# Kernel optimization log

Measured on AMD Instinct MI355X. Metric: run time of the kernel, lower is better.

Reference implementation:

```python
import jax, jax.numpy as jnp
import numpy as np

B, T, D, H = 2, 2048, 2048, 16
HD = D // H  # head_dim = 128
ROPE_THETA = 10000.0


def _apply_rope_interleaved(x, cos, sin):
    # x: (B, T, H, HD); cos/sin: (1, T, 1, HD//2). rope_fraction=1.0, HD even.
    x1 = x[..., ::2]
    x2 = x[..., 1::2]
    rot = jnp.stack([x1 * cos - x2 * sin, x1 * sin + x2 * cos], axis=-1)
    return rot.reshape(x.shape)


def setup_inputs() -> dict:
    key = jax.random.key(0)
    k1, k2, k3 = jax.random.split(key, 3)
    x = jax.random.normal(k1, (B, T, D), dtype=jnp.float32)
    # DenseGeneral qkv kernel: (D, H, 3*HD), lecun_normal-ish scale
    w_qkv = jax.random.normal(k2, (D, H, 3 * HD), dtype=jnp.float32) / np.sqrt(D)
    # out Dense kernel: (D, D)
    w_out = jax.random.normal(k3, (D, D), dtype=jnp.float32) / np.sqrt(D)
    return {"x": x, "w_qkv": w_qkv, "w_out": w_out}


def reference(x, w_qkv, w_out):
    # Fused QKV projection: (B,T,D) x (D,H,3HD) -> (B,T,H,3HD)
    qkv = jnp.einsum("btd,dhf->bthf", x, w_qkv)
    q, k, v = jnp.split(qkv, 3, axis=-1)  # each (B,T,H,HD)

    # RoPE cos/sin at positions arange(T)
    pos = jnp.arange(T, dtype=jnp.float32)
    inv_freq = 1.0 / (ROPE_THETA ** (jnp.arange(0, HD, 2, dtype=jnp.float32) / HD))
    angles = pos[:, None] * inv_freq[None, :]  # (T, HD//2)
    cos = jnp.cos(angles)[None, :, None, :]
    sin = jnp.sin(angles)[None, :, None, :]

    q = _apply_rope_interleaved(q, cos, sin)
    k = _apply_rope_interleaved(k, cos, sin)

    sm_scale = 1.0 / np.sqrt(HD)
    # (B,H,T,HD)
    qh = jnp.transpose(q, (0, 2, 1, 3))
    kh = jnp.transpose(k, (0, 2, 1, 3))
    vh = jnp.transpose(v, (0, 2, 1, 3))

    scores = jnp.einsum("bhqd,bhkd->bhqk", qh, kh) * sm_scale
    causal = jnp.tril(jnp.ones((T, T), dtype=bool))
    scores = jnp.where(causal[None, None], scores, jnp.float32(-1e30))
    probs = jax.nn.softmax(scores, axis=-1)
    yh = jnp.einsum("bhqk,bhkd->bhqd", probs, vh)

    y = jnp.transpose(yh, (0, 2, 1, 3)).reshape(B, T, D)
    # deterministic=True -> dropout is identity; out projection
    return jnp.einsum("btd,de->bte", y, w_out)
```

## Files before the change

### kernel.cpp

```cpp
#include <hip/hip_runtime.h>
#include <math.h>

typedef unsigned short u16;
typedef unsigned int u32;
typedef __attribute__((ext_vector_type(8))) short short8;
typedef __attribute__((ext_vector_type(4))) float f32x4;
typedef __attribute__((ext_vector_type(16))) float f32x16;

#define Bb 2
#define Tt 2048
#define Dd 2048
#define Hh 16
#define HDim 128
#define NQKV 6144
#define CEXP_VAL 0.127521410699097f

__device__ __forceinline__ u16 f2b(float f) {
    u32 u = __float_as_uint(f);
    u32 r = (u + 0x7FFFu + ((u >> 16) & 1u)) >> 16;
    return (u16)r;
}
__device__ __forceinline__ float2 b2f2(u32 u) {
    return make_float2(__uint_as_float(u << 16), __uint_as_float(u & 0xFFFF0000u));
}
__device__ __forceinline__ u32 pack2(float a, float b) {
    return (u32)f2b(a) | ((u32)f2b(b) << 16);
}
__device__ __forceinline__ u32 pack2rz(float a, float b) {
    u32 ua = __float_as_uint(a) + 0x8000u;
    u32 ub = __float_as_uint(b) + 0x8000u;
    return (ua >> 16) | (ub & 0xFFFF0000u);
}

#define GLD16(g, l) __builtin_amdgcn_global_load_lds(                                   \
    (const __attribute__((address_space(1))) void*)(g),                                 \
    (__attribute__((address_space(3))) void*)(l), 16, 0, 0)

__global__ __launch_bounds__(256) void cast_f32_bf16(const float* __restrict__ src,
                                                     u16* __restrict__ dst, int n) {
    int i = (blockIdx.x * 256 + threadIdx.x) * 4;
    if (i >= n) return;
    float4 v = *(const float4*)(src + i);
    *(uint2*)(dst + i) = make_uint2(pack2(v.x, v.y), pack2(v.z, v.w));
}

__global__ __launch_bounds__(256) void transpose_cast(const float* __restrict__ src,
                                                      u16* __restrict__ dst, int R, int C) {
    __shared__ float tile[32][33];
    int c0 = blockIdx.x << 5, r0 = blockIdx.y << 5;
    int tx = threadIdx.x & 31, ty = threadIdx.x >> 5;
    #pragma unroll
    for (int i = 0; i < 32; i += 8)
        tile[ty + i][tx] = src[(size_t)(r0 + ty + i) * C + c0 + tx];
    __syncthreads();
    #pragma unroll
    for (int i = 0; i < 32; i += 8)
        dst[(size_t)(c0 + ty + i) * R + r0 + tx] = f2b(tile[tx][ty + i]);
}

template <int OMODE, int KH>
__global__ __launch_bounds__(256) void gemm_bt(const u16* __restrict__ A, const u16* __restrict__ Bt,
                                               void* __restrict__ Cv, int Mn, int Nn, int Kn) {
    __shared__ __align__(16) u16 As[KH * 4096];
    __shared__ __align__(16) u16 Bs[KH * 4096];
    const int tid = threadIdx.x;
    const int m0 = blockIdx.y << 7, n0 = blockIdx.x << 7;
    const int wave = tid >> 6, lane = tid & 63;
    const int wm = (wave >> 1) << 6, wn = (wave & 1) << 6;
    const int l15 = lane & 15, lq = lane >> 4;

    f32x4 acc[4][4];
    #pragma unroll
    for (int i = 0; i < 4; i++)
        #pragma unroll
        for (int j = 0; j < 4; j++)
            acc[i][j] = (f32x4){0.f, 0.f, 0.f, 0.f};

    const int srow = wave * 32 + (lane >> 2);
    const int scol = (lane & 3) << 3;
    const u16* ga = A + (size_t)(m0 + srow) * Kn + scol;
    const u16* gb = Bt + (size_t)(n0 + srow) * Kn + scol;
    u16* lA = &As[wave * 1024];
    u16* lB = &Bs[wave * 1024];

    for (int k0 = 0; k0 < Kn; k0 += 32 * KH) {
        __syncthreads();
        #pragma unroll
        for (int h = 0; h < KH; h++) {
            GLD16(ga + k0 + h * 32, lA + h * 4096);
            GLD16(ga + k0 + h * 32 + (size_t)16 * Kn, lA + h * 4096 + 512);
            GLD16(gb + k0 + h * 32, lB + h * 4096);
            GLD16(gb + k0 + h * 32 + (size_t)16 * Kn, lB + h * 4096 + 512);
        }
        __syncthreads();
        #pragma unroll
        for (int h = 0; h < KH; h++) {
            const u16* Ah = As + h * 4096;
            const u16* Bh = Bs + h * 4096;
            short8 a[4], b[4];
            #pragma unroll
            for (int i = 0; i < 4; i++) {
                a[i] = *(const short8*)&Ah[(wm + (i << 4) + l15) * 32 + lq * 8];
                b[i] = *(const short8*)&Bh[(wn + (i << 4) + l15) * 32 + lq * 8];
            }
            #pragma unroll
            for (int i = 0; i < 4; i++)
                #pragma unroll
                for (int j = 0; j < 4; j++)
                    acc[i][j] = __builtin_amdgcn_mfma_f32_16x16x32_bf16(a[i], b[j], acc[i][j], 0, 0, 0);
        }
    }

    #pragma unroll
    for (int i = 0; i < 4; i++) {
        int mbase = m0 + wm + (i << 4) + (lq << 2);
        #pragma unroll
        for (int j = 0; j < 4; j++) {
            int n = n0 + wn + (j << 4) + l15;
            if constexpr (OMODE == 1) {
                #pragma unroll
                for (int r = 0; r < 4; r++)
                    ((float*)Cv)[(size_t)(mbase + r) * Nn + n] = acc[i][j][r];
            } else {
                int f = n >> 7;
                int h = f / 3, sel = f - 3 * h;
                int d = n & 127;
                u16* base = (u16*)Cv + (size_t)sel * 8388608;
                #pragma unroll
                for (int r = 0; r < 4; r++) {
                    int m = mbase + r;
                    int b = m >> 11, t = m & 2047;
                    base[(((size_t)(b * 16 + h)) * 2048 + t) * 128 + d] = f2b(acc[i][j][r]);
                }
            }
        }
    }
}

__global__ __launch_bounds__(256) void rope_planar(u16* __restrict__ qk) {
    int gid = blockIdx.x * 256 + threadIdx.x;
    int i = gid & 63;
    int t = (gid >> 6) & 2047;
    int bh = gid >> 17;
    size_t off = ((size_t)bh * 2048 + t) * 128 + 2 * i;
    u16* pq = qk + off;
    u16* pk = qk + 8388608 + off;
    float ang = (float)t * exp2f(-0.20762050596f * (float)i);
    float sv, cv;
    sincosf(ang, &sv, &cv);
    float2 q = b2f2(*(const u32*)pq);
    float2 k = b2f2(*(const u32*)pk);
    *(u32*)pq = pack2((q.x * cv - q.y * sv) * CEXP_VAL, (q.x * sv + q.y * cv) * CEXP_VAL);
    *(u32*)pk = pack2(k.x * cv - k.y * sv, k.x * sv + k.y * cv);
}

__global__ __launch_bounds__(256, 2) void attn_mfma(const u16* __restrict__ qh, const u16* __restrict__ kh,
                                                    const u16* __restrict__ vh, u16* __restrict__ yb) {
    __shared__ __align__(16) u16 smem[17536];
    u16* Ks = smem;
    u16* Vt = smem + 8320;
    u16* Qs = smem;

    const int tid = threadIdx.x;
    const int w = tid >> 6, lane = tid & 63;
    const int l31 = lane & 31, hf = lane >> 5;
    const int bid = blockIdx.x;
    const int bh = bid & 31;
    const int g = bid >> 5;
    const int qt = (g < 8) ? g : 23 - g;
    const u16* qp = qh + (size_t)bh * Tt * HDim;
    const u16* kp = kh + (size_t)bh * Tt * HDim;
    const u16* vp = vh + (size_t)bh * Tt * HDim;
    const int b = bh >> 4, h = bh & 15;
    const int qbase = qt * 128 + w * 32;

    #pragma unroll
    for (int i = 0; i < 8; i++) {
        int p = w * 8 + i;
        GLD16(qp + (size_t)(qt * 128 + p * 4 + (lane >> 4)) * HDim + (lane & 15) * 8,
              &Qs[p * 520]);
    }
    __syncthreads();
    const int qrow = w * 32 + l31;
    short8 qfrag[8];
    #pragma unroll
    for (int kc = 0; kc < 8; kc++)
        qfrag[kc] = *(const short8*)&Qs[(qrow >> 2) * 520 + (qrow & 3) * 128 + kc * 16 + hf * 8];

    float l_i = 0.f;
    f32x16 oacc[4];
    #pragma unroll
    for (int dt = 0; dt < 4; dt++)
        #pragma unroll
        for (int r = 0; r < 16; r++) oacc[dt][r] = 0.f;

    const int vkp = tid & 31, vdc = tid >> 5;
    const int nkt = 2 * qt + 2;
    for (int kt = 0; kt < nkt; kt++) {
        const int k0 = kt << 6;
        __syncthreads();
        #pragma unroll
        for (int i = 0; i < 4; i++) {
            int p = w * 4 + i;
            GLD16(kp + (size_t)(k0 + p * 4 + (lane >> 4)) * HDim + (lane & 15) * 8,
                  &Ks[p * 520]);
        }
        {
            const u16* vsrc = vp + (size_t)(k0 + 2 * vkp) * HDim + vdc * 16;
            uint4 r0a = *(const uint4*)vsrc;
            uint4 r0b = *(const uint4*)(vsrc + 8);
            uint4 r1a = *(const uint4*)(vsrc + HDim);
            uint4 r1b = *(const uint4*)(vsrc + HDim + 8);
            const u16* e0a = (const u16*)&r0a; const u16* e0b = (const u16*)&r0b;
            const u16* e1a = (const u16*)&r1a; const u16* e1b = (const u16*)&r1b;
            #pragma unroll
            for (int j = 0; j < 8; j++)
                *(u32*)&Vt[(vdc * 16 + j) * 72 + vkp * 2] = (u32)e0a[j] | ((u32)e1a[j] << 16);
            #pragma unroll
            for (int j = 0; j < 8; j++)
                *(u32*)&Vt[(vdc * 16 + 8 + j) * 72 + vkp * 2] = (u32)e0b[j] | ((u32)e1b[j] << 16);
        }
        __syncthreads();

        if (k0 <= qbase + 31) {
            float pv[2][16];
            #pragma unroll
            for (int mt = 0; mt < 2; mt++) {
                f32x16 st;
                #pragma unroll
                for (int r = 0; r < 16; r++) st[r] = 0.f;
                const int krow = mt * 32 + l31;
                const u16* kbase = &Ks[(krow >> 2) * 520 + (krow & 3) * 128 + hf * 8];
                #pragma unroll
                for (int kc = 0; kc < 8; kc++) {
                    short8 ka = *(const short8*)(kbase + kc * 16);
                    st = __builtin_amdgcn_mfma_f32_32x32x16_bf16(ka, qfrag[kc], st, 0, 0, 0);
                }
                #pragma unroll
                for (int r = 0; r < 16; r++) pv[mt][r] = st[r];
            }
            const int qg = qbase + l31;
            if (k0 + 63 > qbase) {
                #pragma unroll
                for (int mt = 0; mt < 2; mt++)
                    #pragma unroll
                    for (int r = 0; r < 16; r++) {
                        int kg = k0 + mt * 32 + (r & 3) + 8 * (r >> 2) + 4 * hf;
                        if (kg > qg) pv[mt][r] = -1e30f;
                    }
            }
            #pragma unroll
            for (int mt = 0; mt < 2; mt++)
                #pragma unroll
                for (int r = 0; r < 16; r++) {
                    float p = exp2f(pv[mt][r]);
                    pv[mt][r] = p;
                    l_i += p;
                }

            u32 pu[2][8], px[2][8];
            #pragma unroll
            for (int mt = 0; mt < 2; mt++)
                #pragma unroll
                for (int g2 = 0; g2 < 8; g2++)
                    pu[mt][g2] = pack2rz(pv[mt][2 * g2], pv[mt][2 * g2 + 1]);
            #pragma unroll
            for (int mt = 0; mt < 2; mt++)
                #pragma unroll
                for (int g2 = 0; g2 < 8; g2++)
                    px[mt][g2] = (u32)__shfl_xor((int)pu[mt][g2], 32, 64);
            short8 pb[4];
            #pragma unroll
            for (int kc = 0; kc < 4; kc++) {
                int mt = kc >> 1, g0 = (kc & 1) * 4;
                u32 f[4];
                if (hf == 0) {
                    f[0] = pu[mt][g0]; f[1] = pu[mt][g0 + 1];
                    f[2] = px[mt][g0]; f[3] = px[mt][g0 + 1];
                } else {
                    f[0] = px[mt][g0 + 2]; f[1] = px[mt][g0 + 3];
                    f[2] = pu[mt][g0 + 2]; f[3] = pu[mt][g0 + 3];
                }
                pb[kc] = *(short8*)f;
            }
            #pragma unroll
            for (int dt = 0; dt < 4; dt++) {
                const u16* vbase = &Vt[(dt * 32 + l31) * 72 + hf * 8];
                #pragma unroll
                for (int kc = 0; kc < 4; kc++) {
                    short8 va = *(const short8*)(vbase + kc * 16);
                    oacc[dt] = __builtin_amdgcn_mfma_f32_32x32x16_bf16(va, pb[kc], oacc[dt], 0, 0, 0);
                }
            }
        }
    }

    float l_tot = l_i + __shfl_xor(l_i, 32, 64);
    float linv = 1.0f / l_tot;
    #pragma unroll
    for (int dt = 0; dt < 4; dt++)
        #pragma unroll
        for (int r = 0; r < 16; r++) oacc[dt][r] *= linv;
    __syncthreads();
    u16* E = smem + w * 4384;
    const int rb[8] = {0, 2, 8, 10, 16, 18, 24, 26};
    #pragma unroll
    for (int dt = 0; dt < 4; dt++)
        #pragma unroll
        for (int g2 = 0; g2 < 8; g2++) {
            int d0 = dt * 32 + rb[g2] + 4 * hf;
            *(u32*)&E[l31 * 136 + d0] = pack2(oacc[dt][2 * g2], oacc[dt][2 * g2 + 1]);
        }
    __syncthreads();
    #pragma unroll
    for (int p8 = 0; p8 < 8; p8++) {
        int ql = p8 * 4 + (lane >> 4);
        uint4 ov = *(const uint4*)&E[ql * 136 + (lane & 15) * 8];
        int t = qt * 128 + w * 32 + ql;
        *(uint4*)(yb + ((size_t)(b * Tt + t)) * Dd + h * HDim + (lane & 15) * 8) = ov;
    }
}

extern "C" void kernel_launch(void* const* d_in, const int* in_sizes, int n_in,
                              void* d_out, int out_size, void* d_ws, size_t ws_size,
                              hipStream_t stream) {
    const float* x     = (const float*)d_in[0];
    const float* w_qkv = (const float*)d_in[1];
    const float* w_out = (const float*)d_in[2];
    float* out = (float*)d_out;

    u16* ws    = (u16*)d_ws;
    u16* xb    = ws;
    u16* wqkvT = xb + 8388608;
    u16* woutT = wqkvT + 12582912;
    u16* qhb   = woutT + 4194304;
    u16* khb   = qhb + 8388608;
    u16* vhb   = khb + 8388608;
    u16* yb    = vhb + 8388608;

    cast_f32_bf16<<<8192, 256, 0, stream>>>(x, xb, 8388608);
    transpose_cast<<<dim3(192, 64), 256, 0, stream>>>(w_qkv, wqkvT, 2048, 6144);
    transpose_cast<<<dim3(64, 64), 256, 0, stream>>>(w_out, woutT, 2048, 2048);
    gemm_bt<2, 2><<<dim3(48, 32), 256, 0, stream>>>(xb, wqkvT, (void*)qhb, 4096, 6144, 2048);
    rope_planar<<<16384, 256, 0, stream>>>(qhb);
    attn_mfma<<<512, 256, 0, stream>>>(qhb, khb, vhb, yb);
    gemm_bt<1, 4><<<dim3(16, 32), 256, 0, stream>>>(yb, woutT, (void*)out, 4096, 2048, 2048);
}
```

Before: 396.5 us.

## Double-buffer shared memory in attention and output-projection GEMM to overlap loads

Adds LDS double buffering to the attention kernel: the next K tile is loaded asynchronously and the next V tile is held in registers, then written transposed after the current tile's compute. One barrier per iteration is dropped. The output-projection GEMM becomes a separate double-buffered kernel with 64-wide K steps that prefetches into the alternate buffer. LDS use doubles (about 70KB in attention), which may limit occupancy, and correctness depends on the async global-to-LDS loads having finished when the barrier is reached.

```diff
diff --git a/kernel.cpp b/kernel.cpp
--- a/kernel.cpp
+++ b/kernel.cpp
@@ -58,11 +58,10 @@
         dst[(size_t)(c0 + ty + i) * R + r0 + tx] = f2b(tile[tx][ty + i]);
 }
 
-template <int OMODE, int KH>
-__global__ __launch_bounds__(256) void gemm_bt(const u16* __restrict__ A, const u16* __restrict__ Bt,
-                                               void* __restrict__ Cv, int Mn, int Nn, int Kn) {
-    __shared__ __align__(16) u16 As[KH * 4096];
-    __shared__ __align__(16) u16 Bs[KH * 4096];
+__global__ __launch_bounds__(256) void gemm_qkv(const u16* __restrict__ A, const u16* __restrict__ Bt,
+                                                u16* __restrict__ Cv, int Mn, int Nn, int Kn) {
+    __shared__ __align__(16) u16 As[2 * 4096];
+    __shared__ __align__(16) u16 Bs[2 * 4096];
     const int tid = threadIdx.x;
     const int m0 = blockIdx.y << 7, n0 = blockIdx.x << 7;
     const int wave = tid >> 6, lane = tid & 63;
@@ -83,10 +82,10 @@
     u16* lA = &As[wave * 1024];
     u16* lB = &Bs[wave * 1024];
 
-    for (int k0 = 0; k0 < Kn; k0 += 32 * KH) {
+    for (int k0 = 0; k0 < Kn; k0 += 64) {
         __syncthreads();
         #pragma unroll
-        for (int h = 0; h < KH; h++) {
+        for (int h = 0; h < 2; h++) {
             GLD16(ga + k0 + h * 32, lA + h * 4096);
             GLD16(ga + k0 + h * 32 + (size_t)16 * Kn, lA + h * 4096 + 512);
             GLD16(gb + k0 + h * 32, lB + h * 4096);
@@ -94,7 +93,7 @@
         }
         __syncthreads();
         #pragma unroll
-        for (int h = 0; h < KH; h++) {
+        for (int h = 0; h < 2; h++) {
             const u16* Ah = As + h * 4096;
             const u16* Bh = Bs + h * 4096;
             short8 a[4], b[4];
@@ -117,22 +116,92 @@
         #pragma unroll
         for (int j = 0; j < 4; j++) {
             int n = n0 + wn + (j << 4) + l15;
-            if constexpr (OMODE == 1) {
-                #pragma unroll
-                for (int r = 0; r < 4; r++)
-                    ((float*)Cv)[(size_t)(mbase + r) * Nn + n] = acc[i][j][r];
-            } else {
-                int f = n >> 7;
-                int h = f / 3, sel = f - 3 * h;
-                int d = n & 127;
-                u16* base = (u16*)Cv + (size_t)sel * 8388608;
-                #pragma unroll
-                for (int r = 0; r < 4; r++) {
-                    int m = mbase + r;
-                    int b = m >> 11, t = m & 2047;
-                    base[(((size_t)(b * 16 + h)) * 2048 + t) * 128 + d] = f2b(acc[i][j][r]);
-                }
-            }
+            int f = n >> 7;
+            int h = f / 3, sel = f - 3 * h;
+            int d = n & 127;
+            u16* base = Cv + (size_t)sel * 8388608;
+            #pragma unroll
+            for (int r = 0; r < 4; r++) {
+                int m = mbase + r;
+                int b = m >> 11, t = m & 2047;
+                base[(((size_t)(b * 16 + h)) * 2048 + t) * 128 + d] = f2b(acc[i][j][r]);
+            }
+        }
+    }
+}
+
+__global__ __launch_bounds__(256, 2) void gemm_db(const u16* __restrict__ A, const u16* __restrict__ Bt,
+                                                  float* __restrict__ Cv, int Mn, int Nn, int Kn) {
+    __shared__ __align__(16) u16 As[2 * 8192];
+    __shared__ __align__(16) u16 Bs[2 * 8192];
+    const int tid = threadIdx.x;
+    const int m0 = blockIdx.y << 7, n0 = blockIdx.x << 7;
+    const int wave = tid >> 6, lane = tid & 63;
+    const int wm = (wave >> 1) << 6, wn = (wave & 1) << 6;
+    const int l15 = lane & 15, lq = lane >> 4;
+
+    f32x4 acc[4][4];
+    #pragma unroll
+    for (int i = 0; i < 4; i++)
+        #pragma unroll
+        for (int j = 0; j < 4; j++)
+            acc[i][j] = (f32x4){0.f, 0.f, 0.f, 0.f};
+
+    const int srow = wave * 32 + (lane >> 2);
+    const int scol = (lane & 3) << 3;
+    const u16* ga = A + (size_t)(m0 + srow) * Kn + scol;
+    const u16* gb = Bt + (size_t)(n0 + srow) * Kn + scol;
+    const int lofs = wave * 1024;
+
+    #pragma unroll
+    for (int h = 0; h < 2; h++) {
+        GLD16(ga + h * 32, &As[lofs + h * 4096]);
+        GLD16(ga + h * 32 + (size_t)16 * Kn, &As[lofs + h * 4096 + 512]);
+        GLD16(gb + h * 32, &Bs[lofs + h * 4096]);
+        GLD16(gb + h * 32 + (size_t)16 * Kn, &Bs[lofs + h * 4096 + 512]);
+    }
+
+    for (int k0 = 0; k0 < Kn; k0 += 64) {
+        const int cb = (k0 >> 6) & 1;
+        const int nb = 1 - cb;
+        __syncthreads();
+        if (k0 + 64 < Kn) {
+            const int kn = k0 + 64;
+            #pragma unroll
+            for (int h = 0; h < 2; h++) {
+                GLD16(ga + kn + h * 32, &As[nb * 8192 + lofs + h * 4096]);
+                GLD16(ga + kn + h * 32 + (size_t)16 * Kn, &As[nb * 8192 + lofs + h * 4096 + 512]);
+                GLD16(gb + kn + h * 32, &Bs[nb * 8192 + lofs + h * 4096]);
+                GLD16(gb + kn + h * 32 + (size_t)16 * Kn, &Bs[nb * 8192 + lofs + h * 4096 + 512]);
+            }
+        }
+        #pragma unroll
+        for (int h = 0; h < 2; h++) {
+            const u16* Ah = As + cb * 8192 + h * 4096;
+            const u16* Bh = Bs + cb * 8192 + h * 4096;
+            short8 a[4], b[4];
+            #pragma unroll
+            for (int i = 0; i < 4; i++) {
+                a[i] = *(const short8*)&Ah[(wm + (i << 4) + l15) * 32 + lq * 8];
+                b[i] = *(const short8*)&Bh[(wn + (i << 4) + l15) * 32 + lq * 8];
+            }
+            #pragma unroll
+            for (int i = 0; i < 4; i++)
+                #pragma unroll
+                for (int j = 0; j < 4; j++)
+                    acc[i][j] = __builtin_amdgcn_mfma_f32_16x16x32_bf16(a[i], b[j], acc[i][j], 0, 0, 0);
+        }
+    }
+
+    #pragma unroll
+    for (int i = 0; i < 4; i++) {
+        int mbase = m0 + wm + (i << 4) + (lq << 2);
+        #pragma unroll
+        for (int j = 0; j < 4; j++) {
+            int n = n0 + wn + (j << 4) + l15;
+            #pragma unroll
+            for (int r = 0; r < 4; r++)
+                Cv[(size_t)(mbase + r) * Nn + n] = acc[i][j][r];
         }
     }
 }
@@ -156,9 +225,7 @@
 
 __global__ __launch_bounds__(256, 2) void attn_mfma(const u16* __restrict__ qh, const u16* __restrict__ kh,
                                                     const u16* __restrict__ vh, u16* __restrict__ yb) {
-    __shared__ __align__(16) u16 smem[17536];
-    u16* Ks = smem;
-    u16* Vt = smem + 8320;
+    __shared__ __align__(16) u16 smem[35072];
     u16* Qs = smem;
 
     const int tid = threadIdx.x;
@@ -186,6 +253,7 @@
     #pragma unroll
     for (int kc = 0; kc < 8; kc++)
         qfrag[kc] = *(const short8*)&Qs[(qrow >> 2) * 520 + (qrow & 3) * 128 + kc * 16 + hf * 8];
+    __syncthreads();
 
     float l_i = 0.f;
     f32x16 oacc[4];
@@ -196,31 +264,54 @@
 
     const int vkp = tid & 31, vdc = tid >> 5;
     const int nkt = 2 * qt + 2;
+
+    {
+        #pragma unroll
+        for (int i = 0; i < 4; i++) {
+            int p = w * 4 + i;
+            GLD16(kp + (size_t)(p * 4 + (lane >> 4)) * HDim + (lane & 15) * 8, &smem[p * 520]);
+        }
+        const u16* vsrc = vp + (size_t)(2 * vkp) * HDim + vdc * 16;
+        uint4 r0a = *(const uint4*)vsrc;
+        uint4 r0b = *(const uint4*)(vsrc + 8);
+        uint4 r1a = *(const uint4*)(vsrc + HDim);
+        uint4 r1b = *(const uint4*)(vsrc + HDim + 8);
+        u16* Vt0 = smem + 8320;
+        const u16* e0a = (const u16*)&r0a; const u16* e0b = (const u16*)&r0b;
+        const u16* e1a = (const u16*)&r1a; const u16* e1b = (const u16*)&r1b;
+        #pragma unroll
+        for (int j = 0; j < 8; j++)
+            *(u32*)&Vt0[(vdc * 16 + j) * 72 + vkp * 2] = (u32)e0a[j] | ((u32)e1a[j] << 16);
+        #pragma unroll
+        for (int j = 0; j < 8; j++)
+            *(u32*)&Vt0[(vdc * 16 + 8 + j) * 72 + vkp * 2] = (u32)e0b[j] | ((u32)e1b[j] << 16);
+    }
+
     for (int kt = 0; kt < nkt; kt++) {
         const int k0 = kt << 6;
+        const int cb = kt & 1;
+        u16* Ks = smem + cb * 17536;
+        u16* Vt = Ks + 8320;
         __syncthreads();
-        #pragma unroll
-        for (int i = 0; i < 4; i++) {
-            int p = w * 4 + i;
-            GLD16(kp + (size_t)(k0 + p * 4 + (lane >> 4)) * HDim + (lane & 15) * 8,
-                  &Ks[p * 520]);
-        }
-        {
-            const u16* vsrc = vp + (size_t)(k0 + 2 * vkp) * HDim + vdc * 16;
-            uint4 r0a = *(const uint4*)vsrc;
-            uint4 r0b = *(const uint4*)(vsrc + 8);
-            uint4 r1a = *(const uint4*)(vsrc + HDim);
-            uint4 r1b = *(const uint4*)(vsrc + HDim + 8);
-            const u16* e0a = (const u16*)&r0a; const u16* e0b = (const u16*)&r0b;
-            const u16* e1a = (const u16*)&r1a; const u16* e1b = (const u16*)&r1b;
-            #pragma unroll
-            for (int j = 0; j < 8; j++)
-                *(u32*)&Vt[(vdc * 16 + j) * 72 + vkp * 2] = (u32)e0a[j] | ((u32)e1a[j] << 16);
-            #pragma unroll
-            for (int j = 0; j < 8; j++)
-                *(u32*)&Vt[(vdc * 16 + 8 + j) * 72 + vkp * 2] = (u32)e0b[j] | ((u32)e1b[j] << 16);
-        }
-        __syncthreads();
+
+        uint4 r0a, r0b, r1a, r1b;
+        const bool has_next = (kt + 1 < nkt);
+        u16* VtN = smem + (1 - cb) * 17536 + 8320;
+        if (has_next) {
+            const int kn0 = k0 + 64;
+            u16* KsN = smem + (1 - cb) * 17536;
+            #pragma unroll
+            for (int i = 0; i < 4; i++) {
+                int p = w * 4 + i;
+                GLD16(kp + (size_t)(kn0 + p * 4 + (lane >> 4)) * HDim + (lane & 15) * 8,
+                      &KsN[p * 520]);
+            }
+            const u16* vsrc = vp + (size_t)(kn0 + 2 * vkp) * HDim + vdc * 16;
+            r0a = *(const uint4*)vsrc;
+            r0b = *(const uint4*)(vsrc + 8);
+            r1a = *(const uint4*)(vsrc + HDim);
+            r1b = *(const uint4*)(vsrc + HDim + 8);
+        }
 
         if (k0 <= qbase + 31) {
             float pv[2][16];
@@ -293,6 +384,17 @@
                 }
             }
         }
+
+        if (has_next) {
+            const u16* e0a = (const u16*)&r0a; const u16* e0b = (const u16*)&r0b;
+            const u16* e1a = (const u16*)&r1a; const u16* e1b = (const u16*)&r1b;
+            #pragma unroll
+            for (int j = 0; j < 8; j++)
+                *(u32*)&VtN[(vdc * 16 + j) * 72 + vkp * 2] = (u32)e0a[j] | ((u32)e1a[j] << 16);
+            #pragma unroll
+            for (int j = 0; j < 8; j++)
+                *(u32*)&VtN[(vdc * 16 + 8 + j) * 72 + vkp * 2] = (u32)e0b[j] | ((u32)e1b[j] << 16);
+        }
     }
 
     float l_tot = l_i + __shfl_xor(l_i, 32, 64);
@@ -341,8 +443,8 @@
     cast_f32_bf16<<<8192, 256, 0, stream>>>(x, xb, 8388608);
     transpose_cast<<<dim3(192, 64), 256, 0, stream>>>(w_qkv, wqkvT, 2048, 6144);
     transpose_cast<<<dim3(64, 64), 256, 0, stream>>>(w_out, woutT, 2048, 2048);
-    gemm_bt<2, 2><<<dim3(48, 32), 256, 0, stream>>>(xb, wqkvT, (void*)qhb, 4096, 6144, 2048);
+    gemm_qkv<<<dim3(48, 32), 256, 0, stream>>>(xb, wqkvT, qhb, 4096, 6144, 2048);
     rope_planar<<<16384, 256, 0, stream>>>(qhb);
     attn_mfma<<<512, 256, 0, stream>>>(qhb, khb, vhb, yb);
-    gemm_bt<1, 4><<<dim3(16, 32), 256, 0, stream>>>(yb, woutT, (void*)out, 4096, 2048, 2048);
-}
+    gemm_db<<<dim3(16, 32), 256, 0, stream>>>(yb, woutT, out, 4096, 2048, 2048);
+}
```

Measured after the change: 409.2 us. 3.2% more time.
